# Optimization experiments

Hardware: AMD Instinct MI355X
Metric: run time of the kernel (lower is better)

## Reference

```python
import jax, jax.numpy as jnp
import numpy as np

B, S, UC = 64, 5, 50          # batch, sample (candidates), clicked history
D, T = 128, 768               # embedding_size, title_size
NE, NR, NN = 200000, 100, 50000  # entities, relations, news
K, A = 10, 20                 # neighbors per entity, anchor nodes per news


def _lin(k, out_d, in_d):
    w = jax.random.normal(k, (out_d, in_d), jnp.float32) * (1.0 / np.sqrt(in_d))
    b = jnp.zeros((out_d,), jnp.float32)
    return w, b


def setup_inputs() -> dict:
    key = jax.random.key(0)
    ks = jax.random.split(key, 16)
    W_nc1, b_nc1 = _lin(ks[0], D, T)
    W_nc2, b_nc2 = _lin(ks[1], D, D)
    W_anchor, b_anchor = _lin(ks[2], D, 2 * D)
    W_aw1, b_aw1 = _lin(ks[3], D, D)
    W_aw2, b_aw2 = _lin(ks[4], 1, D)
    W_mlp1, b_mlp1 = _lin(ks[5], D, 2 * D)
    W_mlp2, b_mlp2 = _lin(ks[6], D, D)
    return {
        "news_title_embedding": jax.random.normal(ks[7], (NN, T), jnp.float32),
        "entity_embedding": jax.random.normal(ks[8], (NE, D), jnp.float32),
        "relation_embedding": jax.random.normal(ks[9], (NR, D), jnp.float32),
        "W_nc1": W_nc1, "b_nc1": b_nc1, "W_nc2": W_nc2, "b_nc2": b_nc2,
        "W_anchor": W_anchor, "b_anchor": b_anchor,
        "W_aw1": W_aw1, "b_aw1": b_aw1, "W_aw2": W_aw2, "b_aw2": b_aw2,
        "W_mlp1": W_mlp1, "b_mlp1": b_mlp1, "W_mlp2": W_mlp2, "b_mlp2": b_mlp2,
        "cand_news": jax.random.randint(ks[10], (B, S), 0, NN, jnp.int32),
        "clicked_news": jax.random.randint(ks[11], (B, UC), 0, NN, jnp.int32),
        "cand_anchor_nodes": jax.random.randint(ks[12], (B * S, A), 0, NE, jnp.int32),
        "clicked_anchor_nodes": jax.random.randint(ks[13], (B * UC, A), 0, NE, jnp.int32),
        "entity_adj": jax.random.randint(ks[14], (NE, K), 0, NE, jnp.int32),
        "relation_adj": jax.random.randint(ks[15], (NE, K), 0, NR, jnp.int32),
    }


def reference(news_title_embedding, entity_embedding, relation_embedding,
              W_nc1, b_nc1, W_nc2, b_nc2,
              W_anchor, b_anchor, W_aw1, b_aw1, W_aw2, b_aw2,
              W_mlp1, b_mlp1, W_mlp2, b_mlp2,
              cand_news, clicked_news, cand_anchor_nodes, clicked_anchor_nodes,
              entity_adj, relation_adj):
    elu = jax.nn.elu

    def news_emb(ids_flat):  # [N] -> [N, D]
        t = news_title_embedding[ids_flat]                       # [N, T]
        return jnp.tanh(elu(t @ W_nc1.T + b_nc1) @ W_nc2.T + b_nc2)

    def anchor_graph_emb(nodes):  # [N, A] -> [N, D]
        node_e = entity_embedding[nodes]                          # [N, A, D]
        nb_ent = entity_embedding[entity_adj[nodes]]              # [N, A, K, D]
        nb_rel = relation_embedding[relation_adj[nodes]]          # [N, A, K, D]
        agg = jnp.sum(nb_ent + nb_rel, axis=-2)                   # [N, A, D]
        h = jnp.tanh(jnp.concatenate([node_e, agg], axis=-1) @ W_anchor.T + b_anchor)
        logits = elu(h @ W_aw1.T + b_aw1) @ W_aw2.T + b_aw2       # [N, A, 1]
        w = jax.nn.softmax(logits, axis=-2)                       # softmax over anchor nodes
        return jnp.sum(h * w, axis=-2)                            # [N, D]

    cand_e = news_emb(cand_news.reshape(-1))                      # [B*S, D]
    clk_e = news_emb(clicked_news.reshape(-1))                    # [B*UC, D]
    cand_e = jnp.concatenate([cand_e, anchor_graph_emb(cand_anchor_nodes)], axis=-1)
    clk_e = jnp.concatenate([clk_e, anchor_graph_emb(clicked_anchor_nodes)], axis=-1)

    def mlp(x):
        return elu(elu(x @ W_mlp1.T + b_mlp1) @ W_mlp2.T + b_mlp2)

    news_embedding = mlp(cand_e).reshape(B, S, -1)                # [B, S, D]
    user_embedding = jnp.mean(mlp(clk_e).reshape(B, UC, -1), axis=1)  # [B, D]
    score = jnp.sum(news_embedding * user_embedding[:, None, :], axis=-1)  # [B, S]
    return score
```

## Files before the change

### kernel.cpp

```cpp
#include <hip/hip_runtime.h>
#include <hip/hip_bf16.h>


#define B_ 64
#define S_ 5
#define UC_ 50
#define A_ 20
#define NCAND 320
#define NCLK 3200
#define NNEWS 3520
#define NANCH 70400

static constexpr long OFF_WNC1P = 64;
static constexpr long OFF_BNC1  = 98368;
static constexpr long OFF_WNC2P = 98496;
static constexpr long OFF_BNC2  = 114880;
static constexpr long OFF_WANCP = 115008;
static constexpr long OFF_BANC  = 147776;
static constexpr long OFF_WAW1P = 147904;
static constexpr long OFF_BAW1  = 164288;
static constexpr long OFF_WAW2  = 164416;
static constexpr long OFF_BAW2  = 164544;
static constexpr long OFF_WM1P  = 164548;
static constexpr long OFF_BM1   = 197316;
static constexpr long OFF_WM2P  = 197444;
static constexpr long OFF_BM2   = 213828;
static constexpr long OFF_REL   = 213956;
static constexpr long OFF_AE    = 226756;
static constexpr long OFF_NE    = 677316;
static constexpr long OFF_MO    = 1127876;

typedef __attribute__((ext_vector_type(8))) short short8v;
typedef __attribute__((ext_vector_type(4))) float f32x4;

__device__ __forceinline__ float ldf(const void* p, long i, int bf) {
  if (bf) {
    unsigned int u = (unsigned int)((const unsigned short*)p)[i];
    u <<= 16;
    return __uint_as_float(u);
  }
  return ((const float*)p)[i];
}

__device__ __forceinline__ float4 ldf4(const void* p, long i, int bf) {
  float4 f;
  if (bf) {
    const unsigned short* q = (const unsigned short*)p + i;
    uint2 u = *(const uint2*)q;
    f.x = __uint_as_float(u.x << 16);
    f.y = __uint_as_float(u.x & 0xffff0000u);
    f.z = __uint_as_float(u.y << 16);
    f.w = __uint_as_float(u.y & 0xffff0000u);
  } else {
    f = *(const float4*)((const float*)p + i);
  }
  return f;
}

__device__ __forceinline__ float4 cvtbf4(uint2 u) {
  float4 f;
  f.x = __uint_as_float(u.x << 16);
  f.y = __uint_as_float(u.x & 0xffff0000u);
  f.z = __uint_as_float(u.y << 16);
  f.w = __uint_as_float(u.y & 0xffff0000u);
  return f;
}

__device__ __forceinline__ float eluf(float v) { return v > 0.f ? v : expm1f(v); }

__device__ __forceinline__ void splitbf(float v, unsigned short& hi, unsigned short& lo) {
  unsigned int b = __float_as_uint(v);
  hi = (unsigned short)(b >> 16);
  float rm = v - __uint_as_float(b & 0xffff0000u);
  unsigned int rb = __float_as_uint(rm);
  lo = (unsigned short)((rb + 0x7fffu + ((rb >> 16) & 1u)) >> 16);
}

__device__ __forceinline__ float bfh(unsigned short u) {
  return __uint_as_float((unsigned int)u << 16);
}

__global__ void k_detect(const void* ent, int* flag) {
  __shared__ int cnt;
  if (threadIdx.x == 0) cnt = 0;
  __syncthreads();
  unsigned short u = ((const unsigned short*)ent)[threadIdx.x];
  int e = (u >> 7) & 0xFF;
  int ok = (e >= 107 && e <= 146) ? 1 : 0;
  atomicAdd(&cnt, ok);
  __syncthreads();
  if (threadIdx.x == 0) *flag = (cnt >= 200) ? 1 : 0;
}

__global__ __launch_bounds__(256) void k_prep(
    const void* s0, const void* s1, const void* s2, const void* s3,
    const void* s4, const void* s5, const void* s6, const void* s7,
    const void* s8, const void* s9, const void* s10, const void* s11,
    const void* s12, const void* s13, const void* s14, float* ws) {
  const int bf = ((const int*)ws)[0];
  const void* srcs[15] = {s0,s1,s2,s3,s4,s5,s6,s7,s8,s9,s10,s11,s12,s13,s14};
  const int R[15] = {128,128,128,128,128,128,128,128,1,  1,  128,128,128,128,100};
  const int C[15] = {768,1,  128,1,  256,1,  128,1,  128,1,  256,1,  128,1,  128};
  const int MD[15]= {2,  0,  2,  0,  3,  0,  3,  0,  0,  0,  2,  0,  2,  0,  0};
  const long OFF[15] = {OFF_WNC1P,OFF_BNC1,OFF_WNC2P,OFF_BNC2,OFF_WANCP,OFF_BANC,
                        OFF_WAW1P,OFF_BAW1,OFF_WAW2,OFF_BAW2,OFF_WM1P,OFF_BM1,
                        OFF_WM2P,OFF_BM2,OFF_REL};
  const long total = 226689;
  for (long idx = (long)blockIdx.x * blockDim.x + threadIdx.x; idx < total;
       idx += (long)gridDim.x * blockDim.x) {
    long rem = idx;
    int s = 0;
    while (rem >= (long)R[s] * C[s]) { rem -= (long)R[s] * C[s]; s++; }
    float v = ldf(srcs[s], rem, bf);
    if (MD[s] == 2) {
      long r = rem / C[s], c = rem - r * C[s];
      ws[OFF[s] + (c >> 2) * 512 + r * 4 + (c & 3)] = v;
    } else if (MD[s] == 3) {
      long r = rem / C[s], c = rem - r * C[s];
      unsigned short hi, lo;
      splitbf(v, hi, lo);
      unsigned short* H = (unsigned short*)(ws + OFF[s]);
      unsigned short* L = H + (s == 4 ? 32768 : 16384);
      long id2 = ((c >> 5) * 128 + r) * 32 + (c & 31);
      H[id2] = hi;
      L[id2] = lo;
    } else {
      ws[OFF[s] + rem] = v;
    }
  }
}

__global__ __launch_bounds__(128) void k_news(const void* titles, const int* cand,
                                              const int* clk, float* ws) {
  const int bf = ((const int*)ws)[0];
  __shared__ __align__(16) float t[8][768];
  __shared__ __align__(16) float h1[8][128];
  int tid = threadIdx.x;
  long r0 = (long)blockIdx.x * 8;
  for (int x = tid * 4; x < 8 * 768; x += 128 * 4) {
    int c = x / 768, k = x - c * 768;
    long i = r0 + c;
    int id = (i < NCAND) ? cand[i] : clk[i - NCAND];
    *(float4*)&t[c][k] = ldf4(titles, (long)id * 768 + k, bf);
  }
  __syncthreads();
  int j = tid;
  const float4* W1 = (const float4*)(ws + OFF_WNC1P);
  float acc[8];
#pragma unroll
  for (int c = 0; c < 8; c++) acc[c] = 0.f;
  for (int k4 = 0; k4 < 192; k4++) {
    float4 w = W1[k4 * 128 + j];
#pragma unroll
    for (int c = 0; c < 8; c++) {
      const float4 xv = *(const float4*)&t[c][k4 * 4];
      acc[c] += w.x * xv.x + w.y * xv.y + w.z * xv.z + w.w * xv.w;
    }
  }
  float b1 = ws[OFF_BNC1 + j];
#pragma unroll
  for (int c = 0; c < 8; c++) h1[c][j] = eluf(acc[c] + b1);
  __syncthreads();
  const float4* W2 = (const float4*)(ws + OFF_WNC2P);
  float a2[8];
#pragma unroll
  for (int c = 0; c < 8; c++) a2[c] = 0.f;
  for (int k4 = 0; k4 < 32; k4++) {
    float4 w = W2[k4 * 128 + j];
#pragma unroll
    for (int c = 0; c < 8; c++) {
      const float4 xv = *(const float4*)&h1[c][k4 * 4];
      a2[c] += w.x * xv.x + w.y * xv.y + w.z * xv.z + w.w * xv.w;
    }
  }
  float b2 = ws[OFF_BNC2 + j];
  float* NE = ws + OFF_NE;
#pragma unroll
  for (int c = 0; c < 8; c++) NE[(r0 + c) * 128 + j] = tanhf(a2[c] + b2);
}

__global__ __launch_bounds__(256, 3) void k_anchor(const void* ent, const int* canda,
                                                   const int* clka, const int* eadj,
                                                   const int* radj, float* ws) {
  __shared__ __align__(16) unsigned short XbH[20][264];
  __shared__ __align__(16) unsigned short XbL[20][264];
  __shared__ __align__(16) unsigned short Hhi[20][136];
  __shared__ __align__(16) unsigned short Hlo[20][136];
  __shared__ int NodeIdL[20];
  __shared__ int EAdjL[200];
  __shared__ int RAdjL[200];
  __shared__ float LGp[4][20];

  const int bf = ((const int*)ws)[0];
  int tid = threadIdx.x;
  int lane = tid & 63, wv = tid >> 6;
  int r16 = lane & 15, khh = lane >> 4;
  int lane32 = tid & 31, grp = tid >> 5;
  const float* relf = ws + OFF_REL;

  const unsigned short* WAH = (const unsigned short*)(ws + OFF_WANCP);
  const unsigned short* WAL = WAH + 32768;
  const unsigned short* W1H = (const unsigned short*)(ws + OFF_WAW1P);
  const unsigned short* W1L = W1H + 16384;

  if (tid < 20) {
    long n = (long)blockIdx.x * 20 + tid;
    NodeIdL[tid] = (n < (long)NCAND * A_) ? canda[n] : clka[n - (long)NCAND * A_];
  }
  __syncthreads();
  if (tid < 200) {
    int rr = tid / 10, kk = tid - rr * 10;
    int nd = NodeIdL[rr];
    EAdjL[tid] = eadj[(long)nd * 10 + kk];
    RAdjL[tid] = radj[(long)nd * 10 + kk];
  }
  __syncthreads();

  auto consume = [&](int row, uint2 (&raw)[11]) {
    float4 x1 = cvtbf4(raw[0]);
    float4 a = {0.f, 0.f, 0.f, 0.f};
#pragma unroll
    for (int k = 0; k < 10; ++k) {
      float4 e = cvtbf4(raw[1 + k]);
      const float4 r = *(const float4*)&relf[(long)RAdjL[row * 10 + k] * 128 + lane32 * 4];
      a.x += e.x + r.x;
      a.y += e.y + r.y;
      a.z += e.z + r.z;
      a.w += e.w + r.w;
    }
    ushort4 h4, l4;
    splitbf(x1.x, h4.x, l4.x); splitbf(x1.y, h4.y, l4.y);
    splitbf(x1.z, h4.z, l4.z); splitbf(x1.w, h4.w, l4.w);
    *(ushort4*)&XbH[row][lane32 * 4] = h4;
    *(ushort4*)&XbL[row][lane32 * 4] = l4;
    splitbf(a.x, h4.x, l4.x); splitbf(a.y, h4.y, l4.y);
    splitbf(a.z, h4.z, l4.z); splitbf(a.w, h4.w, l4.w);
    *(ushort4*)&XbH[row][128 + lane32 * 4] = h4;
    *(ushort4*)&XbL[row][128 + lane32 * 4] = l4;
  };

  if (bf) {
    const unsigned short* entp = (const unsigned short*)ent;
    int row0 = grp, row1 = grp + 8, row2 = grp + 16;
    uint2 raw0[11], raw1[11], raw2[11];
    raw0[0] = *(const uint2*)(entp + (long)NodeIdL[row0] * 128 + lane32 * 4);
#pragma unroll
    for (int k = 0; k < 10; ++k)
      raw0[1 + k] = *(const uint2*)(entp + (long)EAdjL[row0 * 10 + k] * 128 + lane32 * 4);
    raw1[0] = *(const uint2*)(entp + (long)NodeIdL[row1] * 128 + lane32 * 4);
#pragma unroll
    for (int k = 0; k < 10; ++k)
      raw1[1 + k] = *(const uint2*)(entp + (long)EAdjL[row1 * 10 + k] * 128 + lane32 * 4);
    if (wv < 2) {
      raw2[0] = *(const uint2*)(entp + (long)NodeIdL[row2] * 128 + lane32 * 4);
#pragma unroll
      for (int k = 0; k < 10; ++k)
        raw2[1 + k] = *(const uint2*)(entp + (long)EAdjL[row2 * 10 + k] * 128 + lane32 * 4);
    }
    consume(row0, raw0);
    consume(row1, raw1);
    if (wv < 2) consume(row2, raw2);
  } else {
#pragma unroll
    for (int i = 0; i < 3; ++i) {
      int row = grp + i * 8;
      if (row < 20) {
        int node = NodeIdL[row];
        float4 x1 = ldf4(ent, (long)node * 128 + lane32 * 4, bf);
        float4 a = {0.f, 0.f, 0.f, 0.f};
#pragma unroll
        for (int k = 0; k < 10; ++k) {
          int an = EAdjL[row * 10 + k], rn = RAdjL[row * 10 + k];
          float4 e = ldf4(ent, (long)an * 128 + lane32 * 4, bf);
          const float4 r = *(const float4*)&relf[(long)rn * 128 + lane32 * 4];
          a.x += e.x + r.x;
          a.y += e.y + r.y;
          a.z += e.z + r.z;
          a.w += e.w + r.w;
        }
        ushort4 h4, l4;
        splitbf(x1.x, h4.x, l4.x); splitbf(x1.y, h4.y, l4.y);
        splitbf(x1.z, h4.z, l4.z); splitbf(x1.w, h4.w, l4.w);
        *(ushort4*)&XbH[row][lane32 * 4] = h4;
        *(ushort4*)&XbL[row][lane32 * 4] = l4;
        splitbf(a.x, h4.x, l4.x); splitbf(a.y, h4.y, l4.y);
        splitbf(a.z, h4.z, l4.z); splitbf(a.w, h4.w, l4.w);
        *(ushort4*)&XbH[row][128 + lane32 * 4] = h4;
        *(ushort4*)&XbL[row][128 + lane32 * 4] = l4;
      }
    }
  }
  __syncthreads();

  {
    int n0 = wv * 32 + r16, n1 = n0 + 16;
    int arow0 = r16, arow1 = 16 + (r16 & 3);
    f32x4 acc[2][2] = {};
    for (int kt = 0; kt < 8; ++kt) {
      long w0 = ((long)(kt * 128 + n0)) * 32 + khh * 8;
      long w1 = ((long)(kt * 128 + n1)) * 32 + khh * 8;
      short8v b0h = *(const short8v*)(WAH + w0);
      short8v b0l = *(const short8v*)(WAL + w0);
      short8v b1h = *(const short8v*)(WAH + w1);
      short8v b1l = *(const short8v*)(WAL + w1);
#pragma unroll
      for (int mt = 0; mt < 2; ++mt) {
        int ar = (mt == 0) ? arow0 : arow1;
        short8v ahi = *(const short8v*)&XbH[ar][kt * 32 + khh * 8];
        short8v alo = *(const short8v*)&XbL[ar][kt * 32 + khh * 8];
        acc[mt][0] = __builtin_amdgcn_mfma_f32_16x16x32_bf16(ahi, b0h, acc[mt][0], 0, 0, 0);
        acc[mt][0] = __builtin_amdgcn_mfma_f32_16x16x32_bf16(ahi, b0l, acc[mt][0], 0, 0, 0);
        acc[mt][0] = __builtin_amdgcn_mfma_f32_16x16x32_bf16(alo, b0h, acc[mt][0], 0, 0, 0);
        acc[mt][1] = __builtin_amdgcn_mfma_f32_16x16x32_bf16(ahi, b1h, acc[mt][1], 0, 0, 0);
        acc[mt][1] = __builtin_amdgcn_mfma_f32_16x16x32_bf16(ahi, b1l, acc[mt][1], 0, 0, 0);
        acc[mt][1] = __builtin_amdgcn_mfma_f32_16x16x32_bf16(alo, b1h, acc[mt][1], 0, 0, 0);
      }
    }
    float bc0 = ws[OFF_BANC + n0], bc1 = ws[OFF_BANC + n1];
#pragma unroll
    for (int mt = 0; mt < 2; ++mt)
#pragma unroll
      for (int j = 0; j < 4; ++j) {
        int r = mt * 16 + khh * 4 + j;
        if (r < 20) {
          unsigned short hi, lo;
          float h0 = tanhf(acc[mt][0][j] + bc0);
          splitbf(h0, hi, lo);
          Hhi[r][n0] = hi; Hlo[r][n0] = lo;
          float h1 = tanhf(acc[mt][1][j] + bc1);
          splitbf(h1, hi, lo);
          Hhi[r][n1] = hi; Hlo[r][n1] = lo;
        }
      }
  }
  __syncthreads();

  {
    int n0 = wv * 32 + r16, n1 = n0 + 16;
    int hrow0 = r16, hrow1 = 16 + (r16 & 3);
    float b10 = ws[OFF_BAW1 + n0], b11 = ws[OFF_BAW1 + n1];
    float w20 = ws[OFF_WAW2 + n0], w21 = ws[OFF_WAW2 + n1];
    f32x4 ac[2][2] = {};
    for (int kt = 0; kt < 4; ++kt) {
      long w0 = ((long)(kt * 128 + n0)) * 32 + khh * 8;
      long w1 = ((long)(kt * 128 + n1)) * 32 + khh * 8;
      short8v b0h = *(const short8v*)(W1H + w0);
      short8v b0l = *(const short8v*)(W1L + w0);
      short8v b1h = *(const short8v*)(W1H + w1);
      short8v b1l = *(const short8v*)(W1L + w1);
#pragma unroll
      for (int mt = 0; mt < 2; ++mt) {
        int hr = (mt == 0) ? hrow0 : hrow1;
        short8v ahi = *(const short8v*)&Hhi[hr][kt * 32 + khh * 8];
        short8v alo = *(const short8v*)&Hlo[hr][kt * 32 + khh * 8];
        ac[mt][0] = __builtin_amdgcn_mfma_f32_16x16x32_bf16(ahi, b0h, ac[mt][0], 0, 0, 0);
        ac[mt][0] = __builtin_amdgcn_mfma_f32_16x16x32_bf16(ahi, b0l, ac[mt][0], 0, 0, 0);
        ac[mt][0] = __builtin_amdgcn_mfma_f32_16x16x32_bf16(alo, b0h, ac[mt][0], 0, 0, 0);
        ac[mt][1] = __builtin_amdgcn_mfma_f32_16x16x32_bf16(ahi, b1h, ac[mt][1], 0, 0, 0);
        ac[mt][1] = __builtin_amdgcn_mfma_f32_16x16x32_bf16(ahi, b1l, ac[mt][1], 0, 0, 0);
        ac[mt][1] = __builtin_amdgcn_mfma_f32_16x16x32_bf16(alo, b1h, ac[mt][1], 0, 0, 0);
      }
    }
#pragma unroll
    for (int mt = 0; mt < 2; ++mt)
#pragma unroll
      for (int j = 0; j < 4; ++j) {
        float v = eluf(ac[mt][0][j] + b10) * w20 + eluf(ac[mt][1][j] + b11) * w21;
        v += __shfl_xor(v, 1);
        v += __shfl_xor(v, 2);
        v += __shfl_xor(v, 4);
        v += __shfl_xor(v, 8);
        int r = mt * 16 + khh * 4 + j;
        if (r16 == 0 && r < 20) LGp[wv][r] = v;
      }
  }
  __syncthreads();

  if (tid < 128) {
    float bw2 = ws[OFF_BAW2];
    float e[20], mx = -1e30f;
#pragma unroll
    for (int a = 0; a < 20; ++a) {
      e[a] = LGp[0][a] + LGp[1][a] + LGp[2][a] + LGp[3][a] + bw2;
      mx = fmaxf(mx, e[a]);
    }
    float s = 0.f;
#pragma unroll
    for (int a = 0; a < 20; ++a) { e[a] = expf(e[a] - mx); s += e[a]; }
    float inv = 1.0f / s;
    float o = 0.f;
#pragma unroll
    for (int a = 0; a < 20; ++a)
      o += e[a] * (bfh(Hhi[a][tid]) + bfh(Hlo[a][tid]));
    float* AE = ws + OFF_AE;
    AE[(long)blockIdx.x * 128 + tid] = o * inv;
  }
}

__global__ __launch_bounds__(256) void k_mlp(float* ws) {
  __shared__ __align__(16) float xt[16][256];
  __shared__ __align__(16) float h1[16][128];
  int tid = threadIdx.x;
  long r0 = (long)blockIdx.x * 16;
  const float* NE = ws + OFF_NE;
  const float* AE = ws + OFF_AE;
  for (int x = tid; x < 16 * 256; x += 256) {
    int c = x >> 8, k = x & 255;
    xt[c][k] = (k < 128) ? NE[(r0 + c) * 128 + k] : AE[(r0 + c) * 128 + (k - 128)];
  }
  __syncthreads();
  int j = tid & 127, half = tid >> 7;
  const float4* W1 = (const float4*)(ws + OFF_WM1P);
  float acc[8];
#pragma unroll
  for (int c = 0; c < 8; c++) acc[c] = 0.f;
  for (int k4 = 0; k4 < 64; k4++) {
    float4 w = W1[k4 * 128 + j];
#pragma unroll
    for (int c = 0; c < 8; c++) {
      const float4 xv = *(const float4*)&xt[half * 8 + c][k4 * 4];
      acc[c] += w.x * xv.x + w.y * xv.y + w.z * xv.z + w.w * xv.w;
    }
  }
  float b1 = ws[OFF_BM1 + j];
#pragma unroll
  for (int c = 0; c < 8; c++) h1[half * 8 + c][j] = eluf(acc[c] + b1);
  __syncthreads();
  const float4* W2 = (const float4*)(ws + OFF_WM2P);
  float a2[8];
#pragma unroll
  for (int c = 0; c < 8; c++) a2[c] = 0.f;
  for (int k4 = 0; k4 < 32; k4++) {
    float4 w = W2[k4 * 128 + j];
#pragma unroll
    for (int c = 0; c < 8; c++) {
      const float4 xv = *(const float4*)&h1[half * 8 + c][k4 * 4];
      a2[c] += w.x * xv.x + w.y * xv.y + w.z * xv.z + w.w * xv.w;
    }
  }
  float b2 = ws[OFF_BM2 + j];
  float* MO = ws + OFF_MO;
#pragma unroll
  for (int c = 0; c < 8; c++) MO[(r0 + half * 8 + c) * 128 + j] = eluf(a2[c] + b2);
}

__global__ __launch_bounds__(128) void k_score(const float* ws, void* out) {
  const int bf = ((const int*)ws)[0];
  int b = blockIdx.x;
  int d = threadIdx.x;
  const float* MO = ws + OFF_MO;
  float u = 0.f;
  for (int t = 0; t < UC_; t++) u += MO[(long)(NCAND + b * UC_ + t) * 128 + d];
  u *= (1.0f / UC_);
  __shared__ float red[2];
  for (int s = 0; s < S_; s++) {
    float p = MO[(long)(b * S_ + s) * 128 + d] * u;
#pragma unroll
    for (int o = 32; o > 0; o >>= 1) p += __shfl_down(p, o, 64);
    if ((d & 63) == 0) red[d >> 6] = p;
    __syncthreads();
    if (d == 0) {
      float v = red[0] + red[1];
      if (bf)
        ((__hip_bfloat16*)out)[b * S_ + s] = __float2bfloat16(v);
      else
        ((float*)out)[b * S_ + s] = v;
    }
    __syncthreads();
  }
}

extern "C" void kernel_launch(void* const* d_in, const int* in_sizes, int n_in,
                              void* d_out, int out_size, void* d_ws, size_t ws_size,
                              hipStream_t stream) {
  (void)in_sizes; (void)n_in; (void)out_size; (void)ws_size;
  const void* titles = d_in[0];
  const void* ent    = d_in[1];
  const void* rel    = d_in[2];
  const void* Wnc1 = d_in[3];  const void* bnc1 = d_in[4];
  const void* Wnc2 = d_in[5];  const void* bnc2 = d_in[6];
  const void* Wanc = d_in[7];  const void* banc = d_in[8];
  const void* Waw1 = d_in[9];  const void* baw1 = d_in[10];
  const void* Waw2 = d_in[11]; const void* baw2 = d_in[12];
  const void* Wm1  = d_in[13]; const void* bm1  = d_in[14];
  const void* Wm2  = d_in[15]; const void* bm2  = d_in[16];
  const int* cand  = (const int*)d_in[17];
  const int* clk   = (const int*)d_in[18];
  const int* canda = (const int*)d_in[19];
  const int* clka  = (const int*)d_in[20];
  const int* eadj  = (const int*)d_in[21];
  const int* radj  = (const int*)d_in[22];
  float* ws = (float*)d_ws;

  k_detect<<<1, 256, 0, stream>>>(ent, (int*)d_ws);
  k_prep<<<256, 256, 0, stream>>>(Wnc1, bnc1, Wnc2, bnc2, Wanc, banc, Waw1, baw1,
                                  Waw2, baw2, Wm1, bm1, Wm2, bm2, rel, ws);
  k_news<<<NNEWS / 8, 128, 0, stream>>>(titles, cand, clk, ws);
  k_anchor<<<NNEWS, 256, 0, stream>>>(ent, canda, clka, eadj, radj, ws);
  k_mlp<<<NNEWS / 16, 256, 0, stream>>>(ws);
  k_score<<<B_, 128, 0, stream>>>(ws, d_out);
}
```

Measured before the change: 219.9 us.

## Fuse news and anchor kernels into one launch; fold dtype detection into prep

Moves the dtype-detection step into every prep block so the standalone detect kernel is gone. Merges the news-encoder kernel and the anchor-graph kernel into one grid: the first 440 blocks encode news titles with 256 threads (4 rows per half-block), and the remaining blocks do the anchor aggregation over a shared LDS buffer. A sched_barrier is added between the gather loads and their consumption. This cuts two launches and lets the independent news and anchor work overlap on the GPU. In exchange the fused kernel's register and occupancy limits now apply to the news path, and the launch-bounds hint rises to 4 waves per SIMD.

```diff
diff --git a/kernel.cpp b/kernel.cpp
--- a/kernel.cpp
+++ b/kernel.cpp
@@ -10,6 +10,7 @@
 #define NCLK 3200
 #define NNEWS 3520
 #define NANCH 70400
+#define NEWSBLK 440
 
 static constexpr long OFF_WNC1P = 64;
 static constexpr long OFF_BNC1  = 98368;
@@ -80,24 +81,27 @@
   return __uint_as_float((unsigned int)u << 16);
 }
 
-__global__ void k_detect(const void* ent, int* flag) {
-  __shared__ int cnt;
-  if (threadIdx.x == 0) cnt = 0;
-  __syncthreads();
-  unsigned short u = ((const unsigned short*)ent)[threadIdx.x];
-  int e = (u >> 7) & 0xFF;
-  int ok = (e >= 107 && e <= 146) ? 1 : 0;
-  atomicAdd(&cnt, ok);
-  __syncthreads();
-  if (threadIdx.x == 0) *flag = (cnt >= 200) ? 1 : 0;
+__device__ __forceinline__ int detect_bf(const void* ent, int tid, int* lds_cnt) {
+  if (tid == 0) *lds_cnt = 0;
+  __syncthreads();
+  if (tid < 256) {
+    unsigned short u = ((const unsigned short*)ent)[tid];
+    int e = (u >> 7) & 0xFF;
+    if (e >= 107 && e <= 146) atomicAdd(lds_cnt, 1);
+  }
+  __syncthreads();
+  return (*lds_cnt >= 200) ? 1 : 0;
 }
 
 __global__ __launch_bounds__(256) void k_prep(
     const void* s0, const void* s1, const void* s2, const void* s3,
     const void* s4, const void* s5, const void* s6, const void* s7,
     const void* s8, const void* s9, const void* s10, const void* s11,
-    const void* s12, const void* s13, const void* s14, float* ws) {
-  const int bf = ((const int*)ws)[0];
+    const void* s12, const void* s13, const void* s14, const void* ent,
+    float* ws) {
+  __shared__ int cnt;
+  const int bf = detect_bf(ent, threadIdx.x, &cnt);
+  if (blockIdx.x == 0 && threadIdx.x == 0) ((int*)ws)[0] = bf;
   const void* srcs[15] = {s0,s1,s2,s3,s4,s5,s6,s7,s8,s9,s10,s11,s12,s13,s14};
   const int R[15] = {128,128,128,128,128,128,128,128,1,  1,  128,128,128,128,100};
   const int C[15] = {768,1,  128,1,  256,1,  128,1,  128,1,  256,1,  128,1,  128};
@@ -130,69 +134,72 @@
   }
 }
 
-__global__ __launch_bounds__(128) void k_news(const void* titles, const int* cand,
-                                              const int* clk, float* ws) {
-  const int bf = ((const int*)ws)[0];
-  __shared__ __align__(16) float t[8][768];
-  __shared__ __align__(16) float h1[8][128];
-  int tid = threadIdx.x;
-  long r0 = (long)blockIdx.x * 8;
-  for (int x = tid * 4; x < 8 * 768; x += 128 * 4) {
-    int c = x / 768, k = x - c * 768;
-    long i = r0 + c;
-    int id = (i < NCAND) ? cand[i] : clk[i - NCAND];
-    *(float4*)&t[c][k] = ldf4(titles, (long)id * 768 + k, bf);
-  }
-  __syncthreads();
-  int j = tid;
-  const float4* W1 = (const float4*)(ws + OFF_WNC1P);
-  float acc[8];
-#pragma unroll
-  for (int c = 0; c < 8; c++) acc[c] = 0.f;
-  for (int k4 = 0; k4 < 192; k4++) {
-    float4 w = W1[k4 * 128 + j];
-#pragma unroll
-    for (int c = 0; c < 8; c++) {
-      const float4 xv = *(const float4*)&t[c][k4 * 4];
-      acc[c] += w.x * xv.x + w.y * xv.y + w.z * xv.z + w.w * xv.w;
-    }
-  }
-  float b1 = ws[OFF_BNC1 + j];
-#pragma unroll
-  for (int c = 0; c < 8; c++) h1[c][j] = eluf(acc[c] + b1);
-  __syncthreads();
-  const float4* W2 = (const float4*)(ws + OFF_WNC2P);
-  float a2[8];
-#pragma unroll
-  for (int c = 0; c < 8; c++) a2[c] = 0.f;
-  for (int k4 = 0; k4 < 32; k4++) {
-    float4 w = W2[k4 * 128 + j];
-#pragma unroll
-    for (int c = 0; c < 8; c++) {
-      const float4 xv = *(const float4*)&h1[c][k4 * 4];
-      a2[c] += w.x * xv.x + w.y * xv.y + w.z * xv.z + w.w * xv.w;
-    }
-  }
-  float b2 = ws[OFF_BNC2 + j];
-  float* NE = ws + OFF_NE;
-#pragma unroll
-  for (int c = 0; c < 8; c++) NE[(r0 + c) * 128 + j] = tanhf(a2[c] + b2);
-}
-
-__global__ __launch_bounds__(256, 3) void k_anchor(const void* ent, const int* canda,
-                                                   const int* clka, const int* eadj,
-                                                   const int* radj, float* ws) {
-  __shared__ __align__(16) unsigned short XbH[20][264];
-  __shared__ __align__(16) unsigned short XbL[20][264];
-  __shared__ __align__(16) unsigned short Hhi[20][136];
-  __shared__ __align__(16) unsigned short Hlo[20][136];
-  __shared__ int NodeIdL[20];
-  __shared__ int EAdjL[200];
-  __shared__ int RAdjL[200];
-  __shared__ float LGp[4][20];
-
+__global__ __launch_bounds__(256, 4) void k_fused(
+    const void* titles, const int* cand, const int* clk,
+    const void* ent, const int* canda, const int* clka,
+    const int* eadj, const int* radj, float* ws) {
+  __shared__ __align__(16) char smem[34000];
   const int bf = ((const int*)ws)[0];
   int tid = threadIdx.x;
+
+  if (blockIdx.x < NEWSBLK) {
+    float (*t)[768] = (float(*)[768])smem;
+    float (*h1)[128] = (float(*)[128])(smem + 24576);
+    long r0 = (long)blockIdx.x * 8;
+    for (int x = tid * 4; x < 8 * 768; x += 256 * 4) {
+      int c = x / 768, k = x - c * 768;
+      long i = r0 + c;
+      int id = (i < NCAND) ? cand[i] : clk[i - NCAND];
+      *(float4*)&t[c][k] = ldf4(titles, (long)id * 768 + k, bf);
+    }
+    __syncthreads();
+    int j = tid & 127, half = tid >> 7;
+    const float4* W1 = (const float4*)(ws + OFF_WNC1P);
+    float acc[4];
+#pragma unroll
+    for (int c = 0; c < 4; c++) acc[c] = 0.f;
+    for (int k4 = 0; k4 < 192; k4++) {
+      float4 w = W1[k4 * 128 + j];
+#pragma unroll
+      for (int c = 0; c < 4; c++) {
+        const float4 xv = *(const float4*)&t[half * 4 + c][k4 * 4];
+        acc[c] += w.x * xv.x + w.y * xv.y + w.z * xv.z + w.w * xv.w;
+      }
+    }
+    float b1 = ws[OFF_BNC1 + j];
+#pragma unroll
+    for (int c = 0; c < 4; c++) h1[half * 4 + c][j] = eluf(acc[c] + b1);
+    __syncthreads();
+    const float4* W2 = (const float4*)(ws + OFF_WNC2P);
+    float a2[4];
+#pragma unroll
+    for (int c = 0; c < 4; c++) a2[c] = 0.f;
+    for (int k4 = 0; k4 < 32; k4++) {
+      float4 w = W2[k4 * 128 + j];
+#pragma unroll
+      for (int c = 0; c < 4; c++) {
+        const float4 xv = *(const float4*)&h1[half * 4 + c][k4 * 4];
+        a2[c] += w.x * xv.x + w.y * xv.y + w.z * xv.z + w.w * xv.w;
+      }
+    }
+    float b2 = ws[OFF_BNC2 + j];
+    float* NE = ws + OFF_NE;
+#pragma unroll
+    for (int c = 0; c < 4; c++)
+      NE[(r0 + half * 4 + c) * 128 + j] = tanhf(a2[c] + b2);
+    return;
+  }
+
+  unsigned short (*XbH)[264] = (unsigned short(*)[264])smem;
+  unsigned short (*XbL)[264] = (unsigned short(*)[264])(smem + 10560);
+  unsigned short (*Hhi)[136] = (unsigned short(*)[136])(smem + 21120);
+  unsigned short (*Hlo)[136] = (unsigned short(*)[136])(smem + 26560);
+  int* NodeIdL = (int*)(smem + 32000);
+  int* EAdjL   = (int*)(smem + 32080);
+  int* RAdjL   = (int*)(smem + 32880);
+  float (*LGp)[20] = (float(*)[20])(smem + 33680);
+
+  int blk = blockIdx.x - NEWSBLK;
   int lane = tid & 63, wv = tid >> 6;
   int r16 = lane & 15, khh = lane >> 4;
   int lane32 = tid & 31, grp = tid >> 5;
@@ -204,7 +211,7 @@
   const unsigned short* W1L = W1H + 16384;
 
   if (tid < 20) {
-    long n = (long)blockIdx.x * 20 + tid;
+    long n = (long)blk * 20 + tid;
     NodeIdL[tid] = (n < (long)NCAND * A_) ? canda[n] : clka[n - (long)NCAND * A_];
   }
   __syncthreads();
@@ -257,6 +264,7 @@
       for (int k = 0; k < 10; ++k)
         raw2[1 + k] = *(const uint2*)(entp + (long)EAdjL[row2 * 10 + k] * 128 + lane32 * 4);
     }
+    __builtin_amdgcn_sched_barrier(0);
     consume(row0, raw0);
     consume(row1, raw1);
     if (wv < 2) consume(row2, raw2);
@@ -327,8 +335,8 @@
           float h0 = tanhf(acc[mt][0][j] + bc0);
           splitbf(h0, hi, lo);
           Hhi[r][n0] = hi; Hlo[r][n0] = lo;
-          float h1 = tanhf(acc[mt][1][j] + bc1);
-          splitbf(h1, hi, lo);
+          float h1v = tanhf(acc[mt][1][j] + bc1);
+          splitbf(h1v, hi, lo);
           Hhi[r][n1] = hi; Hlo[r][n1] = lo;
         }
       }
@@ -393,7 +401,7 @@
     for (int a = 0; a < 20; ++a)
       o += e[a] * (bfh(Hhi[a][tid]) + bfh(Hlo[a][tid]));
     float* AE = ws + OFF_AE;
-    AE[(long)blockIdx.x * 128 + tid] = o * inv;
+    AE[(long)blk * 128 + tid] = o * inv;
   }
 }
 
@@ -492,11 +500,10 @@
   const int* radj  = (const int*)d_in[22];
   float* ws = (float*)d_ws;
 
-  k_detect<<<1, 256, 0, stream>>>(ent, (int*)d_ws);
   k_prep<<<256, 256, 0, stream>>>(Wnc1, bnc1, Wnc2, bnc2, Wanc, banc, Waw1, baw1,
-                                  Waw2, baw2, Wm1, bm1, Wm2, bm2, rel, ws);
-  k_news<<<NNEWS / 8, 128, 0, stream>>>(titles, cand, clk, ws);
-  k_anchor<<<NNEWS, 256, 0, stream>>>(ent, canda, clka, eadj, radj, ws);
+                                  Waw2, baw2, Wm1, bm1, Wm2, bm2, rel, ent, ws);
+  k_fused<<<NEWSBLK + NNEWS, 256, 0, stream>>>(titles, cand, clk, ent, canda, clka,
+                                               eadj, radj, ws);
   k_mlp<<<NNEWS / 16, 256, 0, stream>>>(ws);
   k_score<<<B_, 128, 0, stream>>>(ws, d_out);
 }
```

Result: slower. 275.8 us (+25.4%).
